# Kernel optimization log

Hardware: AMD Instinct MI355X
Metric: run time of the kernel (lower is better)

Reference implementation:

```python
import jax, jax.numpy as jnp
import numpy as np

IN_F = 1024
OUT_F = 2048
BATCH = 1024
LAMBD = 0.2
TOL = 1e-4
MAX_ITERS = 100


def setup_inputs() -> dict:
    key = jax.random.key(0)
    kx, kw = jax.random.split(key)
    x = jax.random.normal(kx, (BATCH, IN_F), dtype=jnp.float32)
    # weight init exactly as in torch __init__: randn then column-wise (dim=0) L2 normalization
    w = jax.random.normal(kw, (OUT_F, IN_F), dtype=jnp.float32)
    w = w / jnp.linalg.norm(w, axis=0)  # norm over out_features, broadcast over columns
    A = w.T  # (in, out)
    M = A.T @ A + jnp.eye(OUT_F, dtype=jnp.float32)  # (out, out)
    M_inv = jnp.linalg.inv(M).T
    return {"x": x, "weight": w, "M_inv": M_inv}


def _softshrink(z, lambd):
    return jnp.sign(z) * jnp.maximum(jnp.abs(z) - lambd, 0.0)


def _basis_pursuit_admm(A_dot_b, M_inv, lambd=LAMBD, tol=TOL, max_iters=MAX_ITERS):
    # Mask-based equivalent of the torch dynamic-resizing loop: solved rows are
    # frozen instead of removed; v_solution captures v at the iteration a row converges.
    B, Mdim = A_dot_b.shape
    z = jnp.zeros((B, Mdim), dtype=A_dot_b.dtype)
    solved0 = jnp.zeros((B,), dtype=bool)
    init = (z, z, z, z, solved0)  # v, u, v_prev, v_solution, solved

    def step(carry, _):
        v, u, v_prev, v_sol, solved = carry
        b_eff = A_dot_b + v - u                      # (B, M)
        xk = b_eff @ M_inv                           # (B, M) @ (M, M)
        v_new = _softshrink(xk + u, lambd)
        u_new = u + xk - v_new
        # negligible_improvement on the updated v vs previous v
        dx = jnp.linalg.norm(v_new - v_prev, axis=1)
        xn = jnp.linalg.norm(v_new, axis=1)
        conv = (dx / xn) < tol
        newly = conv & (~solved)
        v_sol = jnp.where(newly[:, None], v_new, v_sol)
        frozen = solved[:, None]
        v = jnp.where(frozen, v, v_new)
        u = jnp.where(frozen, u, u_new)
        solved = solved | newly
        return (v, u, v, v_sol, solved), None

    (v, u, v_prev, v_sol, solved), _ = jax.lax.scan(step, init, None, length=max_iters)
    # Matches torch: rows still unsolved after max_iters keep their initial zero solution.
    return v_sol


def reference(x, weight, M_inv):
    input_shape = x.shape
    b = jax.lax.stop_gradient(x.reshape(x.shape[0], -1))  # x.detach() in torch
    A_dot_b = b @ weight.T                                 # b.matmul(A) with A = weight.T
    encoded = _basis_pursuit_admm(A_dot_b, M_inv)
    decoded = encoded @ weight
    return encoded, decoded.reshape(input_shape)
```

## Files before the change

### kernel.cpp

```cpp
#include <hip/hip_runtime.h>
#include <math.h>

#define BATCH 1024
#define IN_F  1024
#define OUT_F 2048
#define LAMBD 0.2f
#define TOL   1e-4f
#define MAX_ITERS 100

#define KSPLIT 4
#define KCHUNK (OUT_F / KSPLIT)
#define BSCALE 32.0f
#define BSCALE_INV 0.03125f

typedef _Float16 half8 __attribute__((ext_vector_type(8)));
typedef _Float16 half4 __attribute__((ext_vector_type(4)));
typedef float    floatx16 __attribute__((ext_vector_type(16)));
typedef unsigned char fp8_t;

#define GLOAD_LDS16(g, l) __builtin_amdgcn_global_load_lds(              \
    (const __attribute__((address_space(1))) void*)(g),                  \
    (__attribute__((address_space(3))) void*)(l), 16, 0, 0)

__device__ inline int pk4_fp8(float a, float b, float c, float d) {
    int w = __builtin_amdgcn_cvt_pk_fp8_f32(a, b, 0, false);
    w = __builtin_amdgcn_cvt_pk_fp8_f32(c, d, w, true);
    return w;
}
__device__ inline fp8_t enc_fp8(float a) {
    return (fp8_t)(__builtin_amdgcn_cvt_pk_fp8_f32(a, a, 0, false) & 0xff);
}
__device__ inline void cvt4_fp8(int w, float o[4]) {
    o[0] = __builtin_amdgcn_cvt_f32_fp8(w, 0);
    o[1] = __builtin_amdgcn_cvt_f32_fp8(w, 1);
    o[2] = __builtin_amdgcn_cvt_f32_fp8(w, 2);
    o[3] = __builtin_amdgcn_cvt_f32_fp8(w, 3);
}

#define NB_INIT 2048
#define NB_CX   1024
#define NB_CW   2048
#define NB_TW   2048
#define NB_SB   4096
#define NB_TOTAL (NB_INIT + NB_CX + NB_CW + NB_TW + NB_SB)

__global__ __launch_bounds__(256)
void setup_kernel(const float* __restrict__ x, const float* __restrict__ w,
                  const float* __restrict__ Minv,
                  float4* __restrict__ v16, float4* __restrict__ u16,
                  float4* __restrict__ enc4, int* __restrict__ solved,
                  _Float16* __restrict__ xh, _Float16* __restrict__ wh,
                  _Float16* __restrict__ whT, fp8_t* __restrict__ BhT) {
    const int b = blockIdx.x;
    const int tid = threadIdx.x;
    __shared__ float tile[32][33];

    if (b < NB_INIT) {
        const int idx = b * 256 + tid;
        const float4 z = make_float4(0.f, 0.f, 0.f, 0.f);
        enc4[idx] = z;
        if (idx < BATCH * OUT_F / 8) { v16[idx] = z; u16[idx] = z; }
        if (idx < BATCH) solved[idx] = 0;
        return;
    }
    if (b < NB_INIT + NB_CX) {
        const int i = ((b - NB_INIT) * 256 + tid) * 4;
        const float4 f = *(const float4*)&x[i];
        half4 h;
        h[0] = (_Float16)f.x; h[1] = (_Float16)f.y;
        h[2] = (_Float16)f.z; h[3] = (_Float16)f.w;
        *(half4*)&xh[i] = h;
        return;
    }
    if (b < NB_INIT + NB_CX + NB_CW) {
        const int i = ((b - NB_INIT - NB_CX) * 256 + tid) * 4;
        const float4 f = *(const float4*)&w[i];
        half4 h;
        h[0] = (_Float16)f.x; h[1] = (_Float16)f.y;
        h[2] = (_Float16)f.z; h[3] = (_Float16)f.w;
        *(half4*)&wh[i] = h;
        return;
    }
    if (b < NB_INIT + NB_CX + NB_CW + NB_TW) {
        const int lb = b - NB_INIT - NB_CX - NB_CW;
        const int bx = lb & 31;
        const int by = lb >> 5;
        const int row0 = by * 32;
        const int col0 = bx * 32;
        const int r = tid >> 3;
        const int c4 = (tid & 7) * 4;
        const float4 b4 = *(const float4*)&w[(size_t)(row0 + r) * IN_F + col0 + c4];
        tile[r][c4 + 0] = b4.x; tile[r][c4 + 1] = b4.y;
        tile[r][c4 + 2] = b4.z; tile[r][c4 + 3] = b4.w;
        __syncthreads();
        half4 h;
#pragma unroll
        for (int j = 0; j < 4; ++j) h[j] = (_Float16)tile[c4 + j][r];
        *(half4*)&whT[(size_t)(col0 + r) * OUT_F + row0 + c4] = h;
        return;
    }
    {
        const int lb = b - NB_INIT - NB_CX - NB_CW - NB_TW;
        const int bx = lb & 63;
        const int by = lb >> 6;
        const int k0 = by * 32;
        const int n0 = bx * 32;
        const int r = tid >> 3;
        const int c4 = (tid & 7) * 4;
        const float4 b4 = *(const float4*)&Minv[(size_t)(k0 + r) * OUT_F + n0 + c4];
        tile[r][c4 + 0] = b4.x; tile[r][c4 + 1] = b4.y;
        tile[r][c4 + 2] = b4.z; tile[r][c4 + 3] = b4.w;
        __syncthreads();
        const int wrd = pk4_fp8(tile[c4 + 0][r] * BSCALE, tile[c4 + 1][r] * BSCALE,
                                tile[c4 + 2][r] * BSCALE, tile[c4 + 3][r] * BSCALE);
        *(int*)&BhT[(size_t)(n0 + r) * OUT_F + k0 + c4] = wrd;
    }
}

__global__ __launch_bounds__(256)
void cast_f16_kernel(const float* __restrict__ in, _Float16* __restrict__ out, int n) {
    const int i = (blockIdx.x * 256 + threadIdx.x) * 4;
    if (i < n) {
        const float4 f = *(const float4*)&in[i];
        half4 h;
        h[0] = (_Float16)f.x; h[1] = (_Float16)f.y;
        h[2] = (_Float16)f.z; h[3] = (_Float16)f.w;
        *(half4*)&out[i] = h;
    }
}

__global__ __launch_bounds__(256)
void mfma_nt_ab(const _Float16* __restrict__ A, const _Float16* __restrict__ B,
                fp8_t* __restrict__ Ab8, fp8_t* __restrict__ Ah,
                int N, int K) {
    __shared__ _Float16 sAB[2][8192];
    const int tid = threadIdx.x;
    const int m0 = blockIdx.y * 128;
    const int n0 = blockIdx.x * 128;
    const int wv = tid >> 6, ln = tid & 63;
    const int half = ln >> 5, l31 = ln & 31;
    const int wm = (wv >> 1) * 64, wn = (wv & 1) * 64;
    const int r0 = tid >> 2, koff = (tid & 3) * 8;
    const size_t ga0 = (size_t)(m0 + r0) * K + koff;
    const size_t ga1 = (size_t)(m0 + r0 + 64) * K + koff;
    const size_t gb0 = (size_t)(n0 + r0) * K + koff;
    const size_t gb1 = (size_t)(n0 + r0 + 64) * K + koff;
    const int ldst0 = tid * 8, ldst1 = (256 + tid) * 8;

    floatx16 acc[2][2];
#pragma unroll
    for (int a = 0; a < 2; ++a)
#pragma unroll
        for (int b = 0; b < 2; ++b)
#pragma unroll
            for (int q = 0; q < 16; ++q) acc[a][b][q] = 0.f;

    {
        _Float16* bufA = sAB[0];
        _Float16* bufB = sAB[0] + 4096;
        GLOAD_LDS16(A + ga0, bufA + ldst0);
        GLOAD_LDS16(A + ga1, bufA + ldst1);
        GLOAD_LDS16(B + gb0, bufB + ldst0);
        GLOAD_LDS16(B + gb1, bufB + ldst1);
    }
    __syncthreads();

    const int nsteps = K >> 5;
    for (int s = 0; s < nsteps; ++s) {
        const int cur = s & 1;
        if (s + 1 < nsteps) {
            const int k = (s + 1) * 32;
            _Float16* bufA = sAB[cur ^ 1];
            _Float16* bufB = sAB[cur ^ 1] + 4096;
            GLOAD_LDS16(A + ga0 + k, bufA + ldst0);
            GLOAD_LDS16(A + ga1 + k, bufA + ldst1);
            GLOAD_LDS16(B + gb0 + k, bufB + ldst0);
            GLOAD_LDS16(B + gb1 + k, bufB + ldst1);
        }
        const _Float16* sA = sAB[cur];
        const _Float16* sB = sAB[cur] + 4096;
#pragma unroll
        for (int kk = 0; kk < 2; ++kk) {
            const int ko = kk * 16 + half * 8;
            const half8 a0 = *(const half8*)&sA[(wm + l31) * 32 + ko];
            const half8 a1 = *(const half8*)&sA[(wm + 32 + l31) * 32 + ko];
            const half8 b0 = *(const half8*)&sB[(wn + l31) * 32 + ko];
            const half8 b1 = *(const half8*)&sB[(wn + 32 + l31) * 32 + ko];
            acc[0][0] = __builtin_amdgcn_mfma_f32_32x32x16_f16(a0, b0, acc[0][0], 0, 0, 0);
            acc[0][1] = __builtin_amdgcn_mfma_f32_32x32x16_f16(a0, b1, acc[0][1], 0, 0, 0);
            acc[1][0] = __builtin_amdgcn_mfma_f32_32x32x16_f16(a1, b0, acc[1][0], 0, 0, 0);
            acc[1][1] = __builtin_amdgcn_mfma_f32_32x32x16_f16(a1, b1, acc[1][1], 0, 0, 0);
        }
        __syncthreads();
    }
#pragma unroll
    for (int mm = 0; mm < 2; ++mm)
#pragma unroll
        for (int nn = 0; nn < 2; ++nn) {
            const int col = n0 + wn + nn * 32 + l31;
#pragma unroll
            for (int q = 0; q < 16; ++q) {
                const int row = m0 + wm + mm * 32 + (q & 3) + 8 * (q >> 2) + 4 * half;
                const size_t o = (size_t)row * N + col;
                const fp8_t e = enc_fp8(acc[mm][nn][q]);
                Ab8[o] = e;
                Ah[o] = e;
            }
        }
}

__global__ __launch_bounds__(256)
void mfma_nn_dec(const _Float16* __restrict__ A, const _Float16* __restrict__ B,
                 float* __restrict__ C, int N, int K) {
    __shared__ _Float16 sAB[2][8192];
    const int tid = threadIdx.x;
    const int m0 = blockIdx.y * 128;
    const int n0 = blockIdx.x * 128;
    const int wv = tid >> 6, ln = tid & 63;
    const int half = ln >> 5, l31 = ln & 31;
    const int wm = (wv >> 1) * 64, wn = (wv & 1) * 64;
    const int r0 = tid >> 2, koff = (tid & 3) * 8;
    const size_t ga0 = (size_t)(m0 + r0) * K + koff;
    const size_t ga1 = (size_t)(m0 + r0 + 64) * K + koff;
    const size_t gb0 = (size_t)(n0 + r0) * K + koff;
    const size_t gb1 = (size_t)(n0 + r0 + 64) * K + koff;
    const int ldst0 = tid * 8, ldst1 = (256 + tid) * 8;

    floatx16 acc[2][2];
#pragma unroll
    for (int a = 0; a < 2; ++a)
#pragma unroll
        for (int b = 0; b < 2; ++b)
#pragma unroll
            for (int q = 0; q < 16; ++q) acc[a][b][q] = 0.f;

    {
        _Float16* bufA = sAB[0];
        _Float16* bufB = sAB[0] + 4096;
        GLOAD_LDS16(A + ga0, bufA + ldst0);
        GLOAD_LDS16(A + ga1, bufA + ldst1);
        GLOAD_LDS16(B + gb0, bufB + ldst0);
        GLOAD_LDS16(B + gb1, bufB + ldst1);
    }
    __syncthreads();

    const int nsteps = K >> 5;
    for (int s = 0; s < nsteps; ++s) {
        const int cur = s & 1;
        if (s + 1 < nsteps) {
            const int k = (s + 1) * 32;
            _Float16* bufA = sAB[cur ^ 1];
            _Float16* bufB = sAB[cur ^ 1] + 4096;
            GLOAD_LDS16(A + ga0 + k, bufA + ldst0);
            GLOAD_LDS16(A + ga1 + k, bufA + ldst1);
            GLOAD_LDS16(B + gb0 + k, bufB + ldst0);
            GLOAD_LDS16(B + gb1 + k, bufB + ldst1);
        }
        const _Float16* sA = sAB[cur];
        const _Float16* sB = sAB[cur] + 4096;
#pragma unroll
        for (int kk = 0; kk < 2; ++kk) {
            const int ko = kk * 16 + half * 8;
            const half8 a0 = *(const half8*)&sA[(wm + l31) * 32 + ko];
            const half8 a1 = *(const half8*)&sA[(wm + 32 + l31) * 32 + ko];
            const half8 b0 = *(const half8*)&sB[(wn + l31) * 32 + ko];
            const half8 b1 = *(const half8*)&sB[(wn + 32 + l31) * 32 + ko];
            acc[0][0] = __builtin_amdgcn_mfma_f32_32x32x16_f16(a0, b0, acc[0][0], 0, 0, 0);
            acc[0][1] = __builtin_amdgcn_mfma_f32_32x32x16_f16(a0, b1, acc[0][1], 0, 0, 0);
            acc[1][0] = __builtin_amdgcn_mfma_f32_32x32x16_f16(a1, b0, acc[1][0], 0, 0, 0);
            acc[1][1] = __builtin_amdgcn_mfma_f32_32x32x16_f16(a1, b1, acc[1][1], 0, 0, 0);
        }
        __syncthreads();
    }
#pragma unroll
    for (int mm = 0; mm < 2; ++mm)
#pragma unroll
        for (int nn = 0; nn < 2; ++nn) {
            const int col = n0 + wn + nn * 32 + l31;
#pragma unroll
            for (int q = 0; q < 16; ++q) {
                const int row = m0 + wm + mm * 32 + (q & 3) + 8 * (q >> 2) + 4 * half;
                C[(size_t)row * N + col] = acc[mm][nn][q];
            }
        }
}

__global__ __launch_bounds__(256)
void xk_mfma(const fp8_t* __restrict__ Ah, const fp8_t* __restrict__ BhT,
             fp8_t* __restrict__ xkp, const int* __restrict__ solved) {
    __shared__ fp8_t smem[2][16384];
    const int tid = threadIdx.x;
    const int m0 = blockIdx.y * 128;
    const int n0 = blockIdx.x * 128;
    const int kz = blockIdx.z;
    constexpr size_t P = (size_t)BATCH * OUT_F;

    __shared__ int s_active;
    if (tid == 0) s_active = 0;
    __syncthreads();
    if (tid < 128 && solved[m0 + tid] == 0) s_active = 1;
    __syncthreads();
    if (!s_active) return;

    const int wv = tid >> 6;
    const int ln = tid & 63;
    const int half = ln >> 5;
    const int l31 = ln & 31;
    const int wm = (wv >> 1) * 64;
    const int wn = (wv & 1) * 64;

    const int r = tid & 127;
    const int c0 = tid >> 7;
    const fp8_t* gA = Ah  + (size_t)(m0 + r) * OUT_F + kz * KCHUNK;
    const fp8_t* gB = BhT + (size_t)(n0 + r) * OUT_F + kz * KCHUNK;
    const int dA0 = (c0 * 128 + r) * 16;
    const int dA1 = ((c0 + 2) * 128 + r) * 16;

    floatx16 acc[2][2];
#pragma unroll
    for (int a = 0; a < 2; ++a)
#pragma unroll
        for (int b = 0; b < 2; ++b)
#pragma unroll
            for (int q = 0; q < 16; ++q) acc[a][b][q] = 0.f;

    const int ao0 = (wm + l31) * 16 + half * 8;
    const int ao1 = (wm + 32 + l31) * 16 + half * 8;
    const int bo0 = (wn + l31) * 16 + half * 8;
    const int bo1 = (wn + 32 + l31) * 16 + half * 8;

    {
        fp8_t* sA = smem[0];
        fp8_t* sB = smem[0] + 8192;
        GLOAD_LDS16(gA + c0 * 16, sA + dA0);
        GLOAD_LDS16(gA + (c0 + 2) * 16, sA + dA1);
        GLOAD_LDS16(gB + c0 * 16, sB + dA0);
        GLOAD_LDS16(gB + (c0 + 2) * 16, sB + dA1);
    }
    __syncthreads();

#pragma unroll 1
    for (int s = 0; s < KCHUNK / 64; ++s) {
        const int cur = s & 1;
        if (s + 1 < KCHUNK / 64) {
            const int k = (s + 1) * 64;
            fp8_t* nA = smem[cur ^ 1];
            fp8_t* nB = smem[cur ^ 1] + 8192;
            GLOAD_LDS16(gA + k + c0 * 16, nA + dA0);
            GLOAD_LDS16(gA + k + (c0 + 2) * 16, nA + dA1);
            GLOAD_LDS16(gB + k + c0 * 16, nB + dA0);
            GLOAD_LDS16(gB + k + (c0 + 2) * 16, nB + dA1);
        }
        const fp8_t* sA = smem[cur];
        const fp8_t* sB = smem[cur] + 8192;
#pragma unroll
        for (int kk = 0; kk < 4; ++kk) {
            const int cb = kk * 2048;
            const long long a0 = *(const long long*)&sA[cb + ao0];
            const long long a1 = *(const long long*)&sA[cb + ao1];
            const long long b0 = *(const long long*)&sB[cb + bo0];
            const long long b1 = *(const long long*)&sB[cb + bo1];
            acc[0][0] = __builtin_amdgcn_mfma_f32_32x32x16_fp8_fp8(a0, b0, acc[0][0], 0, 0, 0);
            acc[0][1] = __builtin_amdgcn_mfma_f32_32x32x16_fp8_fp8(a0, b1, acc[0][1], 0, 0, 0);
            acc[1][0] = __builtin_amdgcn_mfma_f32_32x32x16_fp8_fp8(a1, b0, acc[1][0], 0, 0, 0);
            acc[1][1] = __builtin_amdgcn_mfma_f32_32x32x16_fp8_fp8(a1, b1, acc[1][1], 0, 0, 0);
        }
        __syncthreads();
    }

    fp8_t* sm = smem[0];
#pragma unroll
    for (int mm = 0; mm < 2; ++mm)
#pragma unroll
        for (int nn = 0; nn < 2; ++nn) {
            const int lcol = wn + nn * 32 + l31;
#pragma unroll
            for (int q = 0; q < 16; ++q) {
                const int lrow = wm + mm * 32 + (q & 3) + 8 * (q >> 2) + 4 * half;
                sm[lrow * 128 + lcol] = enc_fp8(acc[mm][nn][q] * BSCALE_INV);
            }
        }
    __syncthreads();
    fp8_t* outp = xkp + kz * P + (size_t)m0 * OUT_F + n0;
#pragma unroll
    for (int s4 = 0; s4 < 4; ++s4) {
        const int f = (s4 * 256 + tid) * 16;
        *(int4*)&outp[(size_t)(f >> 7) * OUT_F + (f & 127)] = *(const int4*)&sm[f];
    }
}

__global__ __launch_bounds__(256)
void update_kernel(const fp8_t* __restrict__ xkp, const fp8_t* __restrict__ Ab8,
                   _Float16* __restrict__ v, _Float16* __restrict__ u,
                   float* __restrict__ enc, fp8_t* __restrict__ Ah,
                   int* __restrict__ solved) {
    const int row = blockIdx.x;
    if (solved[row]) return;
    const int t = threadIdx.x;
    constexpr size_t P = (size_t)BATCH * OUT_F;

    const int c = t * 8;
    const size_t off = (size_t)row * OUT_F + c;
    const int2 q0 = *(const int2*)&xkp[off];
    const int2 q1 = *(const int2*)&xkp[P + off];
    const int2 q2 = *(const int2*)&xkp[2 * P + off];
    const int2 q3 = *(const int2*)&xkp[3 * P + off];
    const half8 u8 = *(const half8*)&u[off];
    const half8 v8 = *(const half8*)&v[off];
    const int2 ab2 = *(const int2*)&Ab8[off];

    float f0[4], f1[4], f2[4], f3[4], g0[4], g1[4], g2[4], g3[4];
    cvt4_fp8(q0.x, f0); cvt4_fp8(q1.x, f1); cvt4_fp8(q2.x, f2); cvt4_fp8(q3.x, f3);
    cvt4_fp8(q0.y, g0); cvt4_fp8(q1.y, g1); cvt4_fp8(q2.y, g2); cvt4_fp8(q3.y, g3);
    float ab0[4], ab1[4];
    cvt4_fp8(ab2.x, ab0); cvt4_fp8(ab2.y, ab1);
    float xs[8], abv[8];
#pragma unroll
    for (int j = 0; j < 4; ++j) {
        xs[j] = f0[j] + f1[j] + f2[j] + f3[j];
        xs[j + 4] = g0[j] + g1[j] + g2[j] + g3[j];
        abv[j] = ab0[j];
        abv[j + 4] = ab1[j];
    }

    float vn_all[8], ae[8];
    half8 vo, uo;
    float dx2 = 0.f, xn2 = 0.f;
#pragma unroll
    for (int j = 0; j < 8; ++j) {
        const float xk = xs[j];
        const float uv = (float)u8[j];
        const float vp = (float)v8[j];
        const float z = xk + uv;
        const float az = fabsf(z) - LAMBD;
        const float vnew = az > 0.f ? copysignf(az, z) : 0.f;
        const float unew = uv + xk - vnew;
        const float d = vnew - vp;
        dx2 += d * d;
        xn2 += vnew * vnew;
        vn_all[j] = vnew;
        vo[j] = (_Float16)vnew;
        uo[j] = (_Float16)unew;
        ae[j] = abv[j] + vnew - unew;
    }
    *(half8*)&v[off] = vo;
    *(half8*)&u[off] = uo;
    int2 ah;
    ah.x = pk4_fp8(ae[0], ae[1], ae[2], ae[3]);
    ah.y = pk4_fp8(ae[4], ae[5], ae[6], ae[7]);
    *(int2*)&Ah[off] = ah;

#pragma unroll
    for (int o = 32; o > 0; o >>= 1) {
        dx2 += __shfl_down(dx2, o);
        xn2 += __shfl_down(xn2, o);
    }
    __shared__ float sdx[4], sxn[4];
    __shared__ float s_conv;
    if ((t & 63) == 0) { sdx[t >> 6] = dx2; sxn[t >> 6] = xn2; }
    __syncthreads();
    if (t == 0) {
        const float dxt = sqrtf(sdx[0] + sdx[1] + sdx[2] + sdx[3]);
        const float xnt = sqrtf(sxn[0] + sxn[1] + sxn[2] + sxn[3]);
        const bool conv = (dxt / xnt) < TOL;
        s_conv = conv ? 1.f : 0.f;
        if (conv) solved[row] = 1;
    }
    __syncthreads();
    if (s_conv != 0.f) {
        *(float4*)&enc[off] = make_float4(vn_all[0], vn_all[1], vn_all[2], vn_all[3]);
        *(float4*)&enc[off + 4] = make_float4(vn_all[4], vn_all[5], vn_all[6], vn_all[7]);
    }
}

extern "C" void kernel_launch(void* const* d_in, const int* in_sizes, int n_in,
                              void* d_out, int out_size, void* d_ws, size_t ws_size,
                              hipStream_t stream) {
    (void)in_sizes; (void)n_in; (void)out_size; (void)ws_size;
    const float* x    = (const float*)d_in[0];
    const float* w    = (const float*)d_in[1];
    const float* Minv = (const float*)d_in[2];

    float* enc = (float*)d_out;
    float* dec = enc + (size_t)BATCH * OUT_F;

    constexpr size_t P = (size_t)BATCH * OUT_F;
    fp8_t* Ab8 = (fp8_t*)d_ws;
    _Float16* v   = (_Float16*)(Ab8 + P);
    _Float16* u   = v + P;
    _Float16* xh  = u + P;
    _Float16* wh  = xh + (size_t)BATCH * IN_F;
    _Float16* whT = wh + (size_t)OUT_F * IN_F;
    _Float16* ench = whT + (size_t)IN_F * OUT_F;
    fp8_t* Ah  = (fp8_t*)(ench + P);
    fp8_t* xkp = Ah + P;
    fp8_t* BhT = xkp + 4 * P;
    int* solved = (int*)(BhT + (size_t)OUT_F * OUT_F);

    setup_kernel<<<NB_TOTAL, 256, 0, stream>>>(
        x, w, Minv, (float4*)v, (float4*)u, (float4*)enc, solved,
        xh, wh, whT, BhT);

    mfma_nt_ab<<<dim3(OUT_F / 128, BATCH / 128), 256, 0, stream>>>(
        xh, wh, Ab8, Ah, OUT_F, IN_F);

    for (int it = 0; it < MAX_ITERS; ++it) {
        xk_mfma<<<dim3(OUT_F / 128, BATCH / 128, KSPLIT), 256, 0, stream>>>(
            Ah, BhT, xkp, solved);
        update_kernel<<<BATCH, 256, 0, stream>>>(xkp, Ab8, v, u, enc, Ah, solved);
    }

    cast_f16_kernel<<<(BATCH * OUT_F / 4 + 255) / 256, 256, 0, stream>>>(enc, ench, BATCH * OUT_F);
    mfma_nn_dec<<<dim3(IN_F / 128, BATCH / 128), 256, 0, stream>>>(
        ench, whT, dec, IN_F, OUT_F);
}
```

Baseline: 2.313 ms.

## Use 512-thread blocks with single-buffered LDS in the MFMA GEMM kernels

The three MFMA GEMM kernels (initial A·b, the per-iteration xk split-K GEMM, and decode) now run with 8 waves per block instead of 4. Each wave computes a 64x32 sub-tile with two accumulators rather than 64x64 with four, and the LDS double buffer is replaced by one buffer with a barrier before and after each load. The aim is more waves in flight to hide latency, and fewer registers and less shared memory per block. In exchange, global loads no longer overlap with MFMA work, each step takes two barriers, and each wave reuses fewer LDS fragments per load.

```diff
diff --git a/kernel.cpp b/kernel.cpp
--- a/kernel.cpp
+++ b/kernel.cpp
@@ -129,166 +129,112 @@
     }
 }
 
-__global__ __launch_bounds__(256)
+__global__ __launch_bounds__(512)
 void mfma_nt_ab(const _Float16* __restrict__ A, const _Float16* __restrict__ B,
                 fp8_t* __restrict__ Ab8, fp8_t* __restrict__ Ah,
                 int N, int K) {
-    __shared__ _Float16 sAB[2][8192];
+    __shared__ _Float16 sA[128 * 32];
+    __shared__ _Float16 sB[128 * 32];
     const int tid = threadIdx.x;
     const int m0 = blockIdx.y * 128;
     const int n0 = blockIdx.x * 128;
     const int wv = tid >> 6, ln = tid & 63;
     const int half = ln >> 5, l31 = ln & 31;
-    const int wm = (wv >> 1) * 64, wn = (wv & 1) * 64;
+    const int wm = (wv >> 2) * 64, wn = (wv & 3) * 32;
     const int r0 = tid >> 2, koff = (tid & 3) * 8;
     const size_t ga0 = (size_t)(m0 + r0) * K + koff;
-    const size_t ga1 = (size_t)(m0 + r0 + 64) * K + koff;
     const size_t gb0 = (size_t)(n0 + r0) * K + koff;
-    const size_t gb1 = (size_t)(n0 + r0 + 64) * K + koff;
-    const int ldst0 = tid * 8, ldst1 = (256 + tid) * 8;
-
-    floatx16 acc[2][2];
+    const int ldst = tid * 8;
+
+    floatx16 acc[2];
 #pragma unroll
     for (int a = 0; a < 2; ++a)
 #pragma unroll
-        for (int b = 0; b < 2; ++b)
-#pragma unroll
-            for (int q = 0; q < 16; ++q) acc[a][b][q] = 0.f;
-
-    {
-        _Float16* bufA = sAB[0];
-        _Float16* bufB = sAB[0] + 4096;
-        GLOAD_LDS16(A + ga0, bufA + ldst0);
-        GLOAD_LDS16(A + ga1, bufA + ldst1);
-        GLOAD_LDS16(B + gb0, bufB + ldst0);
-        GLOAD_LDS16(B + gb1, bufB + ldst1);
-    }
-    __syncthreads();
-
-    const int nsteps = K >> 5;
-    for (int s = 0; s < nsteps; ++s) {
-        const int cur = s & 1;
-        if (s + 1 < nsteps) {
-            const int k = (s + 1) * 32;
-            _Float16* bufA = sAB[cur ^ 1];
-            _Float16* bufB = sAB[cur ^ 1] + 4096;
-            GLOAD_LDS16(A + ga0 + k, bufA + ldst0);
-            GLOAD_LDS16(A + ga1 + k, bufA + ldst1);
-            GLOAD_LDS16(B + gb0 + k, bufB + ldst0);
-            GLOAD_LDS16(B + gb1 + k, bufB + ldst1);
-        }
-        const _Float16* sA = sAB[cur];
-        const _Float16* sB = sAB[cur] + 4096;
+        for (int q = 0; q < 16; ++q) acc[a][q] = 0.f;
+
+    for (int k = 0; k < K; k += 32) {
+        __syncthreads();
+        GLOAD_LDS16(A + ga0 + k, sA + ldst);
+        GLOAD_LDS16(B + gb0 + k, sB + ldst);
+        __syncthreads();
 #pragma unroll
         for (int kk = 0; kk < 2; ++kk) {
             const int ko = kk * 16 + half * 8;
             const half8 a0 = *(const half8*)&sA[(wm + l31) * 32 + ko];
             const half8 a1 = *(const half8*)&sA[(wm + 32 + l31) * 32 + ko];
             const half8 b0 = *(const half8*)&sB[(wn + l31) * 32 + ko];
-            const half8 b1 = *(const half8*)&sB[(wn + 32 + l31) * 32 + ko];
-            acc[0][0] = __builtin_amdgcn_mfma_f32_32x32x16_f16(a0, b0, acc[0][0], 0, 0, 0);
-            acc[0][1] = __builtin_amdgcn_mfma_f32_32x32x16_f16(a0, b1, acc[0][1], 0, 0, 0);
-            acc[1][0] = __builtin_amdgcn_mfma_f32_32x32x16_f16(a1, b0, acc[1][0], 0, 0, 0);
-            acc[1][1] = __builtin_amdgcn_mfma_f32_32x32x16_f16(a1, b1, acc[1][1], 0, 0, 0);
-        }
-        __syncthreads();
-    }
-#pragma unroll
-    for (int mm = 0; mm < 2; ++mm)
-#pragma unroll
-        for (int nn = 0; nn < 2; ++nn) {
-            const int col = n0 + wn + nn * 32 + l31;
-#pragma unroll
-            for (int q = 0; q < 16; ++q) {
-                const int row = m0 + wm + mm * 32 + (q & 3) + 8 * (q >> 2) + 4 * half;
-                const size_t o = (size_t)row * N + col;
-                const fp8_t e = enc_fp8(acc[mm][nn][q]);
-                Ab8[o] = e;
-                Ah[o] = e;
-            }
-        }
-}
-
-__global__ __launch_bounds__(256)
+            acc[0] = __builtin_amdgcn_mfma_f32_32x32x16_f16(a0, b0, acc[0], 0, 0, 0);
+            acc[1] = __builtin_amdgcn_mfma_f32_32x32x16_f16(a1, b0, acc[1], 0, 0, 0);
+        }
+    }
+#pragma unroll
+    for (int mm = 0; mm < 2; ++mm) {
+        const int col = n0 + wn + l31;
+#pragma unroll
+        for (int q = 0; q < 16; ++q) {
+            const int row = m0 + wm + mm * 32 + (q & 3) + 8 * (q >> 2) + 4 * half;
+            const size_t o = (size_t)row * N + col;
+            const fp8_t e = enc_fp8(acc[mm][q]);
+            Ab8[o] = e;
+            Ah[o] = e;
+        }
+    }
+}
+
+__global__ __launch_bounds__(512)
 void mfma_nn_dec(const _Float16* __restrict__ A, const _Float16* __restrict__ B,
                  float* __restrict__ C, int N, int K) {
-    __shared__ _Float16 sAB[2][8192];
+    __shared__ _Float16 sA[128 * 32];
+    __shared__ _Float16 sB[128 * 32];
     const int tid = threadIdx.x;
     const int m0 = blockIdx.y * 128;
     const int n0 = blockIdx.x * 128;
     const int wv = tid >> 6, ln = tid & 63;
     const int half = ln >> 5, l31 = ln & 31;
-    const int wm = (wv >> 1) * 64, wn = (wv & 1) * 64;
+    const int wm = (wv >> 2) * 64, wn = (wv & 3) * 32;
     const int r0 = tid >> 2, koff = (tid & 3) * 8;
     const size_t ga0 = (size_t)(m0 + r0) * K + koff;
-    const size_t ga1 = (size_t)(m0 + r0 + 64) * K + koff;
     const size_t gb0 = (size_t)(n0 + r0) * K + koff;
-    const size_t gb1 = (size_t)(n0 + r0 + 64) * K + koff;
-    const int ldst0 = tid * 8, ldst1 = (256 + tid) * 8;
-
-    floatx16 acc[2][2];
+    const int ldst = tid * 8;
+
+    floatx16 acc[2];
 #pragma unroll
     for (int a = 0; a < 2; ++a)
 #pragma unroll
-        for (int b = 0; b < 2; ++b)
-#pragma unroll
-            for (int q = 0; q < 16; ++q) acc[a][b][q] = 0.f;
-
-    {
-        _Float16* bufA = sAB[0];
-        _Float16* bufB = sAB[0] + 4096;
-        GLOAD_LDS16(A + ga0, bufA + ldst0);
-        GLOAD_LDS16(A + ga1, bufA + ldst1);
-        GLOAD_LDS16(B + gb0, bufB + ldst0);
-        GLOAD_LDS16(B + gb1, bufB + ldst1);
-    }
-    __syncthreads();
-
-    const int nsteps = K >> 5;
-    for (int s = 0; s < nsteps; ++s) {
-        const int cur = s & 1;
-        if (s + 1 < nsteps) {
-            const int k = (s + 1) * 32;
-            _Float16* bufA = sAB[cur ^ 1];
-            _Float16* bufB = sAB[cur ^ 1] + 4096;
-            GLOAD_LDS16(A + ga0 + k, bufA + ldst0);
-            GLOAD_LDS16(A + ga1 + k, bufA + ldst1);
-            GLOAD_LDS16(B + gb0 + k, bufB + ldst0);
-            GLOAD_LDS16(B + gb1 + k, bufB + ldst1);
-        }
-        const _Float16* sA = sAB[cur];
-        const _Float16* sB = sAB[cur] + 4096;
+        for (int q = 0; q < 16; ++q) acc[a][q] = 0.f;
+
+    for (int k = 0; k < K; k += 32) {
+        __syncthreads();
+        GLOAD_LDS16(A + ga0 + k, sA + ldst);
+        GLOAD_LDS16(B + gb0 + k, sB + ldst);
+        __syncthreads();
 #pragma unroll
         for (int kk = 0; kk < 2; ++kk) {
             const int ko = kk * 16 + half * 8;
             const half8 a0 = *(const half8*)&sA[(wm + l31) * 32 + ko];
             const half8 a1 = *(const half8*)&sA[(wm + 32 + l31) * 32 + ko];
             const half8 b0 = *(const half8*)&sB[(wn + l31) * 32 + ko];
-            const half8 b1 = *(const half8*)&sB[(wn + 32 + l31) * 32 + ko];
-            acc[0][0] = __builtin_amdgcn_mfma_f32_32x32x16_f16(a0, b0, acc[0][0], 0, 0, 0);
-            acc[0][1] = __builtin_amdgcn_mfma_f32_32x32x16_f16(a0, b1, acc[0][1], 0, 0, 0);
-            acc[1][0] = __builtin_amdgcn_mfma_f32_32x32x16_f16(a1, b0, acc[1][0], 0, 0, 0);
-            acc[1][1] = __builtin_amdgcn_mfma_f32_32x32x16_f16(a1, b1, acc[1][1], 0, 0, 0);
-        }
-        __syncthreads();
-    }
-#pragma unroll
-    for (int mm = 0; mm < 2; ++mm)
-#pragma unroll
-        for (int nn = 0; nn < 2; ++nn) {
-            const int col = n0 + wn + nn * 32 + l31;
-#pragma unroll
-            for (int q = 0; q < 16; ++q) {
-                const int row = m0 + wm + mm * 32 + (q & 3) + 8 * (q >> 2) + 4 * half;
-                C[(size_t)row * N + col] = acc[mm][nn][q];
-            }
-        }
-}
-
-__global__ __launch_bounds__(256)
+            acc[0] = __builtin_amdgcn_mfma_f32_32x32x16_f16(a0, b0, acc[0], 0, 0, 0);
+            acc[1] = __builtin_amdgcn_mfma_f32_32x32x16_f16(a1, b0, acc[1], 0, 0, 0);
+        }
+    }
+#pragma unroll
+    for (int mm = 0; mm < 2; ++mm) {
+        const int col = n0 + wn + l31;
+#pragma unroll
+        for (int q = 0; q < 16; ++q) {
+            const int row = m0 + wm + mm * 32 + (q & 3) + 8 * (q >> 2) + 4 * half;
+            C[(size_t)row * N + col] = acc[mm][q];
+        }
+    }
+}
+
+__global__ __launch_bounds__(512)
 void xk_mfma(const fp8_t* __restrict__ Ah, const fp8_t* __restrict__ BhT,
              fp8_t* __restrict__ xkp, const int* __restrict__ solved) {
-    __shared__ fp8_t smem[2][16384];
+    __shared__ fp8_t smem[16384];
+    fp8_t* sA = smem;
+    fp8_t* sB = smem + 8192;
     const int tid = threadIdx.x;
     const int m0 = blockIdx.y * 128;
     const int n0 = blockIdx.x * 128;
@@ -306,86 +252,58 @@
     const int ln = tid & 63;
     const int half = ln >> 5;
     const int l31 = ln & 31;
-    const int wm = (wv >> 1) * 64;
-    const int wn = (wv & 1) * 64;
+    const int wm = (wv >> 2) * 64;
+    const int wn = (wv & 3) * 32;
 
     const int r = tid & 127;
     const int c0 = tid >> 7;
     const fp8_t* gA = Ah  + (size_t)(m0 + r) * OUT_F + kz * KCHUNK;
     const fp8_t* gB = BhT + (size_t)(n0 + r) * OUT_F + kz * KCHUNK;
-    const int dA0 = (c0 * 128 + r) * 16;
-    const int dA1 = ((c0 + 2) * 128 + r) * 16;
-
-    floatx16 acc[2][2];
+    const int dst = (c0 * 128 + r) * 16;
+
+    floatx16 acc[2];
 #pragma unroll
     for (int a = 0; a < 2; ++a)
 #pragma unroll
-        for (int b = 0; b < 2; ++b)
-#pragma unroll
-            for (int q = 0; q < 16; ++q) acc[a][b][q] = 0.f;
+        for (int q = 0; q < 16; ++q) acc[a][q] = 0.f;
 
     const int ao0 = (wm + l31) * 16 + half * 8;
     const int ao1 = (wm + 32 + l31) * 16 + half * 8;
     const int bo0 = (wn + l31) * 16 + half * 8;
-    const int bo1 = (wn + 32 + l31) * 16 + half * 8;
-
-    {
-        fp8_t* sA = smem[0];
-        fp8_t* sB = smem[0] + 8192;
-        GLOAD_LDS16(gA + c0 * 16, sA + dA0);
-        GLOAD_LDS16(gA + (c0 + 2) * 16, sA + dA1);
-        GLOAD_LDS16(gB + c0 * 16, sB + dA0);
-        GLOAD_LDS16(gB + (c0 + 2) * 16, sB + dA1);
-    }
-    __syncthreads();
-
-#pragma unroll 1
-    for (int s = 0; s < KCHUNK / 64; ++s) {
-        const int cur = s & 1;
-        if (s + 1 < KCHUNK / 64) {
-            const int k = (s + 1) * 64;
-            fp8_t* nA = smem[cur ^ 1];
-            fp8_t* nB = smem[cur ^ 1] + 8192;
-            GLOAD_LDS16(gA + k + c0 * 16, nA + dA0);
-            GLOAD_LDS16(gA + k + (c0 + 2) * 16, nA + dA1);
-            GLOAD_LDS16(gB + k + c0 * 16, nB + dA0);
-            GLOAD_LDS16(gB + k + (c0 + 2) * 16, nB + dA1);
-        }
-        const fp8_t* sA = smem[cur];
-        const fp8_t* sB = smem[cur] + 8192;
+
+    for (int k = 0; k < KCHUNK; k += 64) {
+        __syncthreads();
+        GLOAD_LDS16(gA + k + c0 * 16, sA + dst);
+        GLOAD_LDS16(gB + k + c0 * 16, sB + dst);
+        __syncthreads();
+
 #pragma unroll
         for (int kk = 0; kk < 4; ++kk) {
             const int cb = kk * 2048;
             const long long a0 = *(const long long*)&sA[cb + ao0];
             const long long a1 = *(const long long*)&sA[cb + ao1];
             const long long b0 = *(const long long*)&sB[cb + bo0];
-            const long long b1 = *(const long long*)&sB[cb + bo1];
-            acc[0][0] = __builtin_amdgcn_mfma_f32_32x32x16_fp8_fp8(a0, b0, acc[0][0], 0, 0, 0);
-            acc[0][1] = __builtin_amdgcn_mfma_f32_32x32x16_fp8_fp8(a0, b1, acc[0][1], 0, 0, 0);
-            acc[1][0] = __builtin_amdgcn_mfma_f32_32x32x16_fp8_fp8(a1, b0, acc[1][0], 0, 0, 0);
-            acc[1][1] = __builtin_amdgcn_mfma_f32_32x32x16_fp8_fp8(a1, b1, acc[1][1], 0, 0, 0);
-        }
-        __syncthreads();
-    }
-
-    fp8_t* sm = smem[0];
-#pragma unroll
-    for (int mm = 0; mm < 2; ++mm)
-#pragma unroll
-        for (int nn = 0; nn < 2; ++nn) {
-            const int lcol = wn + nn * 32 + l31;
-#pragma unroll
-            for (int q = 0; q < 16; ++q) {
-                const int lrow = wm + mm * 32 + (q & 3) + 8 * (q >> 2) + 4 * half;
-                sm[lrow * 128 + lcol] = enc_fp8(acc[mm][nn][q] * BSCALE_INV);
-            }
-        }
+            acc[0] = __builtin_amdgcn_mfma_f32_32x32x16_fp8_fp8(a0, b0, acc[0], 0, 0, 0);
+            acc[1] = __builtin_amdgcn_mfma_f32_32x32x16_fp8_fp8(a1, b0, acc[1], 0, 0, 0);
+        }
+    }
+
+    __syncthreads();
+#pragma unroll
+    for (int mm = 0; mm < 2; ++mm) {
+        const int lcol = wn + l31;
+#pragma unroll
+        for (int q = 0; q < 16; ++q) {
+            const int lrow = wm + mm * 32 + (q & 3) + 8 * (q >> 2) + 4 * half;
+            smem[lrow * 128 + lcol] = enc_fp8(acc[mm][q] * BSCALE_INV);
+        }
+    }
     __syncthreads();
     fp8_t* outp = xkp + kz * P + (size_t)m0 * OUT_F + n0;
 #pragma unroll
-    for (int s4 = 0; s4 < 4; ++s4) {
-        const int f = (s4 * 256 + tid) * 16;
-        *(int4*)&outp[(size_t)(f >> 7) * OUT_F + (f & 127)] = *(const int4*)&sm[f];
+    for (int s4 = 0; s4 < 2; ++s4) {
+        const int f = (s4 * 512 + tid) * 16;
+        *(int4*)&outp[(size_t)(f >> 7) * OUT_F + (f & 127)] = *(const int4*)&smem[f];
     }
 }
 
@@ -501,16 +419,16 @@
         x, w, Minv, (float4*)v, (float4*)u, (float4*)enc, solved,
         xh, wh, whT, BhT);
 
-    mfma_nt_ab<<<dim3(OUT_F / 128, BATCH / 128), 256, 0, stream>>>(
+    mfma_nt_ab<<<dim3(OUT_F / 128, BATCH / 128), 512, 0, stream>>>(
         xh, wh, Ab8, Ah, OUT_F, IN_F);
 
     for (int it = 0; it < MAX_ITERS; ++it) {
-        xk_mfma<<<dim3(OUT_F / 128, BATCH / 128, KSPLIT), 256, 0, stream>>>(
+        xk_mfma<<<dim3(OUT_F / 128, BATCH / 128, KSPLIT), 512, 0, stream>>>(
             Ah, BhT, xkp, solved);
         update_kernel<<<BATCH, 256, 0, stream>>>(xkp, Ab8, v, u, enc, Ah, solved);
     }
 
     cast_f16_kernel<<<(BATCH * OUT_F / 4 + 255) / 256, 256, 0, stream>>>(enc, ench, BATCH * OUT_F);
-    mfma_nn_dec<<<dim3(IN_F / 128, BATCH / 128), 256, 0, stream>>>(
+    mfma_nn_dec<<<dim3(IN_F / 128, BATCH / 128), 512, 0, stream>>>(
         ench, whT, dec, IN_F, OUT_F);
 }
```

Measured after the change: 2.315 ms. About the same (+0.1%).

## Fuse ADMM matmul and update into one kernel with deferred convergence check

Applied to the files above, without the earlier changes.

Merges the split-K FP8 matmul and the per-row update into one kernel. Each 128x128 tile now covers the full K range and applies softshrink, the u/v updates and the next A operand directly from an LDS float tile. This removes the fp8 partial-sum round trip through global memory and one launch per iteration. Row convergence norms become per-tile partials in a ping-pong buffer that the next iteration checks, plus a finalize kernel and a zeroing cast for unsolved rows. The cost is only 128 blocks with no split-K, a single-buffered K loop with two barriers per step, and enc written on every iteration.

```diff
diff --git a/kernel.cpp b/kernel.cpp
--- a/kernel.cpp
+++ b/kernel.cpp
@@ -8,10 +8,9 @@
 #define TOL   1e-4f
 #define MAX_ITERS 100
 
-#define KSPLIT 4
-#define KCHUNK (OUT_F / KSPLIT)
 #define BSCALE 32.0f
 #define BSCALE_INV 0.03125f
+#define PNHALF (BATCH * 32)
 
 typedef _Float16 half8 __attribute__((ext_vector_type(8)));
 typedef _Float16 half4 __attribute__((ext_vector_type(4)));
@@ -49,6 +48,7 @@
                   const float* __restrict__ Minv,
                   float4* __restrict__ v16, float4* __restrict__ u16,
                   float4* __restrict__ enc4, int* __restrict__ solved,
+                  float4* __restrict__ pn4,
                   _Float16* __restrict__ xh, _Float16* __restrict__ wh,
                   _Float16* __restrict__ whT, fp8_t* __restrict__ BhT) {
     const int b = blockIdx.x;
@@ -61,6 +61,7 @@
         enc4[idx] = z;
         if (idx < BATCH * OUT_F / 8) { v16[idx] = z; u16[idx] = z; }
         if (idx < BATCH) solved[idx] = 0;
+        if (idx < 2 * PNHALF / 4) pn4[idx] = z;
         return;
     }
     if (b < NB_INIT + NB_CX) {
@@ -118,22 +119,10 @@
 }
 
 __global__ __launch_bounds__(256)
-void cast_f16_kernel(const float* __restrict__ in, _Float16* __restrict__ out, int n) {
-    const int i = (blockIdx.x * 256 + threadIdx.x) * 4;
-    if (i < n) {
-        const float4 f = *(const float4*)&in[i];
-        half4 h;
-        h[0] = (_Float16)f.x; h[1] = (_Float16)f.y;
-        h[2] = (_Float16)f.z; h[3] = (_Float16)f.w;
-        *(half4*)&out[i] = h;
-    }
-}
-
-__global__ __launch_bounds__(256)
 void mfma_nt_ab(const _Float16* __restrict__ A, const _Float16* __restrict__ B,
                 fp8_t* __restrict__ Ab8, fp8_t* __restrict__ Ah,
                 int N, int K) {
-    __shared__ _Float16 sAB[2][8192];
+    __shared__ _Float16 smem[2][8192];
     const int tid = threadIdx.x;
     const int m0 = blockIdx.y * 128;
     const int n0 = blockIdx.x * 128;
@@ -155,30 +144,26 @@
 #pragma unroll
             for (int q = 0; q < 16; ++q) acc[a][b][q] = 0.f;
 
-    {
-        _Float16* bufA = sAB[0];
-        _Float16* bufB = sAB[0] + 4096;
-        GLOAD_LDS16(A + ga0, bufA + ldst0);
-        GLOAD_LDS16(A + ga1, bufA + ldst1);
-        GLOAD_LDS16(B + gb0, bufB + ldst0);
-        GLOAD_LDS16(B + gb1, bufB + ldst1);
-    }
+    GLOAD_LDS16(A + ga0, smem[0] + ldst0);
+    GLOAD_LDS16(A + ga1, smem[0] + ldst1);
+    GLOAD_LDS16(B + gb0, smem[0] + 4096 + ldst0);
+    GLOAD_LDS16(B + gb1, smem[0] + 4096 + ldst1);
     __syncthreads();
 
-    const int nsteps = K >> 5;
-    for (int s = 0; s < nsteps; ++s) {
-        const int cur = s & 1;
-        if (s + 1 < nsteps) {
+    const int NS = K >> 5;
+#pragma unroll 1
+    for (int s = 0; s < NS; ++s) {
+        if (s + 1 < NS) {
+            _Float16* nb = smem[(s & 1) ^ 1];
             const int k = (s + 1) * 32;
-            _Float16* bufA = sAB[cur ^ 1];
-            _Float16* bufB = sAB[cur ^ 1] + 4096;
-            GLOAD_LDS16(A + ga0 + k, bufA + ldst0);
-            GLOAD_LDS16(A + ga1 + k, bufA + ldst1);
-            GLOAD_LDS16(B + gb0 + k, bufB + ldst0);
-            GLOAD_LDS16(B + gb1 + k, bufB + ldst1);
-        }
-        const _Float16* sA = sAB[cur];
-        const _Float16* sB = sAB[cur] + 4096;
+            GLOAD_LDS16(A + ga0 + k, nb + ldst0);
+            GLOAD_LDS16(A + ga1 + k, nb + ldst1);
+            GLOAD_LDS16(B + gb0 + k, nb + 4096 + ldst0);
+            GLOAD_LDS16(B + gb1 + k, nb + 4096 + ldst1);
+        }
+        __syncthreads();
+        const _Float16* sA = smem[s & 1];
+        const _Float16* sB = smem[s & 1] + 4096;
 #pragma unroll
         for (int kk = 0; kk < 2; ++kk) {
             const int ko = kk * 16 + half * 8;
@@ -212,7 +197,7 @@
 __global__ __launch_bounds__(256)
 void mfma_nn_dec(const _Float16* __restrict__ A, const _Float16* __restrict__ B,
                  float* __restrict__ C, int N, int K) {
-    __shared__ _Float16 sAB[2][8192];
+    __shared__ _Float16 smem[2][8192];
     const int tid = threadIdx.x;
     const int m0 = blockIdx.y * 128;
     const int n0 = blockIdx.x * 128;
@@ -234,30 +219,26 @@
 #pragma unroll
             for (int q = 0; q < 16; ++q) acc[a][b][q] = 0.f;
 
-    {
-        _Float16* bufA = sAB[0];
-        _Float16* bufB = sAB[0] + 4096;
-        GLOAD_LDS16(A + ga0, bufA + ldst0);
-        GLOAD_LDS16(A + ga1, bufA + ldst1);
-        GLOAD_LDS16(B + gb0, bufB + ldst0);
-        GLOAD_LDS16(B + gb1, bufB + ldst1);
-    }
+    GLOAD_LDS16(A + ga0, smem[0] + ldst0);
+    GLOAD_LDS16(A + ga1, smem[0] + ldst1);
+    GLOAD_LDS16(B + gb0, smem[0] + 4096 + ldst0);
+    GLOAD_LDS16(B + gb1, smem[0] + 4096 + ldst1);
     __syncthreads();
 
-    const int nsteps = K >> 5;
-    for (int s = 0; s < nsteps; ++s) {
-        const int cur = s & 1;
-        if (s + 1 < nsteps) {
+    const int NS = K >> 5;
+#pragma unroll 1
+    for (int s = 0; s < NS; ++s) {
+        if (s + 1 < NS) {
+            _Float16* nb = smem[(s & 1) ^ 1];
             const int k = (s + 1) * 32;
-            _Float16* bufA = sAB[cur ^ 1];
-            _Float16* bufB = sAB[cur ^ 1] + 4096;
-            GLOAD_LDS16(A + ga0 + k, bufA + ldst0);
-            GLOAD_LDS16(A + ga1 + k, bufA + ldst1);
-            GLOAD_LDS16(B + gb0 + k, bufB + ldst0);
-            GLOAD_LDS16(B + gb1 + k, bufB + ldst1);
-        }
-        const _Float16* sA = sAB[cur];
-        const _Float16* sB = sAB[cur] + 4096;
+            GLOAD_LDS16(A + ga0 + k, nb + ldst0);
+            GLOAD_LDS16(A + ga1 + k, nb + ldst1);
+            GLOAD_LDS16(B + gb0 + k, nb + 4096 + ldst0);
+            GLOAD_LDS16(B + gb1 + k, nb + 4096 + ldst1);
+        }
+        __syncthreads();
+        const _Float16* sA = smem[s & 1];
+        const _Float16* sB = smem[s & 1] + 4096;
 #pragma unroll
         for (int kk = 0; kk < 2; ++kk) {
             const int ko = kk * 16 + half * 8;
@@ -286,19 +267,45 @@
 }
 
 __global__ __launch_bounds__(256)
-void xk_mfma(const fp8_t* __restrict__ Ah, const fp8_t* __restrict__ BhT,
-             fp8_t* __restrict__ xkp, const int* __restrict__ solved) {
-    __shared__ fp8_t smem[2][16384];
+void fused_iter(const fp8_t* __restrict__ AhCur, fp8_t* __restrict__ AhNxt,
+                const fp8_t* __restrict__ BhT, const fp8_t* __restrict__ Ab8,
+                _Float16* __restrict__ v, _Float16* __restrict__ u,
+                float* __restrict__ enc, int* __restrict__ solved,
+                const float* __restrict__ pnPrev, float* __restrict__ pnCur) {
+    __shared__ __align__(16) fp8_t smem[65536];
+    __shared__ int s_flags[128];
+    __shared__ int s_active;
+
     const int tid = threadIdx.x;
-    const int m0 = blockIdx.y * 128;
-    const int n0 = blockIdx.x * 128;
-    const int kz = blockIdx.z;
-    constexpr size_t P = (size_t)BATCH * OUT_F;
-
-    __shared__ int s_active;
+    const int bx = blockIdx.x;
+    const int by = blockIdx.y;
+    const int m0 = by * 128;
+    const int n0 = bx * 128;
+
     if (tid == 0) s_active = 0;
     __syncthreads();
-    if (tid < 128 && solved[m0 + tid] == 0) s_active = 1;
+    if (tid < 128) {
+        const int row = m0 + tid;
+        int act = 0;
+        if (solved[row] == 0) {
+            const float* pp = pnPrev + row * 32;
+            float dx2 = 0.f, xn2 = 0.f;
+#pragma unroll
+            for (int j = 0; j < 16; ++j) { dx2 += pp[2 * j]; xn2 += pp[2 * j + 1]; }
+            const bool conv = (sqrtf(dx2) / sqrtf(xn2)) < TOL;
+            if (conv) {
+                solved[row] = 1;
+                const int4* src = (const int4*)(AhCur + (size_t)row * OUT_F + n0);
+                int4* dst = (int4*)(AhNxt + (size_t)row * OUT_F + n0);
+#pragma unroll
+                for (int j = 0; j < 8; ++j) dst[j] = src[j];
+            } else {
+                act = 1;
+                s_active = 1;
+            }
+        }
+        s_flags[tid] = act;
+    }
     __syncthreads();
     if (!s_active) return;
 
@@ -311,10 +318,12 @@
 
     const int r = tid & 127;
     const int c0 = tid >> 7;
-    const fp8_t* gA = Ah  + (size_t)(m0 + r) * OUT_F + kz * KCHUNK;
-    const fp8_t* gB = BhT + (size_t)(n0 + r) * OUT_F + kz * KCHUNK;
-    const int dA0 = (c0 * 128 + r) * 16;
-    const int dA1 = ((c0 + 2) * 128 + r) * 16;
+    const fp8_t* gA = AhCur + (size_t)(m0 + r) * OUT_F;
+    const fp8_t* gB = BhT + (size_t)(n0 + r) * OUT_F;
+    const int d0 = ((c0 + 0) * 128 + r) * 16;
+    const int d1 = ((c0 + 2) * 128 + r) * 16;
+    const int d2 = ((c0 + 4) * 128 + r) * 16;
+    const int d3 = ((c0 + 6) * 128 + r) * 16;
 
     floatx16 acc[2][2];
 #pragma unroll
@@ -329,46 +338,35 @@
     const int bo0 = (wn + l31) * 16 + half * 8;
     const int bo1 = (wn + 32 + l31) * 16 + half * 8;
 
-    {
-        fp8_t* sA = smem[0];
-        fp8_t* sB = smem[0] + 8192;
-        GLOAD_LDS16(gA + c0 * 16, sA + dA0);
-        GLOAD_LDS16(gA + (c0 + 2) * 16, sA + dA1);
-        GLOAD_LDS16(gB + c0 * 16, sB + dA0);
-        GLOAD_LDS16(gB + (c0 + 2) * 16, sB + dA1);
-    }
-    __syncthreads();
-
 #pragma unroll 1
-    for (int s = 0; s < KCHUNK / 64; ++s) {
-        const int cur = s & 1;
-        if (s + 1 < KCHUNK / 64) {
-            const int k = (s + 1) * 64;
-            fp8_t* nA = smem[cur ^ 1];
-            fp8_t* nB = smem[cur ^ 1] + 8192;
-            GLOAD_LDS16(gA + k + c0 * 16, nA + dA0);
-            GLOAD_LDS16(gA + k + (c0 + 2) * 16, nA + dA1);
-            GLOAD_LDS16(gB + k + c0 * 16, nB + dA0);
-            GLOAD_LDS16(gB + k + (c0 + 2) * 16, nB + dA1);
-        }
-        const fp8_t* sA = smem[cur];
-        const fp8_t* sB = smem[cur] + 8192;
-#pragma unroll
-        for (int kk = 0; kk < 4; ++kk) {
+    for (int kb = 0; kb < OUT_F / 128; ++kb) {
+        const int ko = kb * 128;
+        __syncthreads();
+        GLOAD_LDS16(gA + ko + (c0 + 0) * 16, smem + d0);
+        GLOAD_LDS16(gA + ko + (c0 + 2) * 16, smem + d1);
+        GLOAD_LDS16(gA + ko + (c0 + 4) * 16, smem + d2);
+        GLOAD_LDS16(gA + ko + (c0 + 6) * 16, smem + d3);
+        GLOAD_LDS16(gB + ko + (c0 + 0) * 16, smem + 16384 + d0);
+        GLOAD_LDS16(gB + ko + (c0 + 2) * 16, smem + 16384 + d1);
+        GLOAD_LDS16(gB + ko + (c0 + 4) * 16, smem + 16384 + d2);
+        GLOAD_LDS16(gB + ko + (c0 + 6) * 16, smem + 16384 + d3);
+        __syncthreads();
+#pragma unroll
+        for (int kk = 0; kk < 8; ++kk) {
             const int cb = kk * 2048;
-            const long long a0 = *(const long long*)&sA[cb + ao0];
-            const long long a1 = *(const long long*)&sA[cb + ao1];
-            const long long b0 = *(const long long*)&sB[cb + bo0];
-            const long long b1 = *(const long long*)&sB[cb + bo1];
+            const long long a0 = *(const long long*)&smem[cb + ao0];
+            const long long a1 = *(const long long*)&smem[cb + ao1];
+            const long long b0 = *(const long long*)&smem[16384 + cb + bo0];
+            const long long b1 = *(const long long*)&smem[16384 + cb + bo1];
             acc[0][0] = __builtin_amdgcn_mfma_f32_32x32x16_fp8_fp8(a0, b0, acc[0][0], 0, 0, 0);
             acc[0][1] = __builtin_amdgcn_mfma_f32_32x32x16_fp8_fp8(a0, b1, acc[0][1], 0, 0, 0);
             acc[1][0] = __builtin_amdgcn_mfma_f32_32x32x16_fp8_fp8(a1, b0, acc[1][0], 0, 0, 0);
             acc[1][1] = __builtin_amdgcn_mfma_f32_32x32x16_fp8_fp8(a1, b1, acc[1][1], 0, 0, 0);
         }
-        __syncthreads();
-    }
-
-    fp8_t* sm = smem[0];
+    }
+
+    __syncthreads();
+    float* ftile = (float*)smem;
 #pragma unroll
     for (int mm = 0; mm < 2; ++mm)
 #pragma unroll
@@ -377,100 +375,92 @@
 #pragma unroll
             for (int q = 0; q < 16; ++q) {
                 const int lrow = wm + mm * 32 + (q & 3) + 8 * (q >> 2) + 4 * half;
-                sm[lrow * 128 + lcol] = enc_fp8(acc[mm][nn][q] * BSCALE_INV);
+                ftile[lrow * 128 + (lcol ^ (lrow & 31))] = acc[mm][nn][q] * BSCALE_INV;
             }
         }
     __syncthreads();
-    fp8_t* outp = xkp + kz * P + (size_t)m0 * OUT_F + n0;
-#pragma unroll
-    for (int s4 = 0; s4 < 4; ++s4) {
-        const int f = (s4 * 256 + tid) * 16;
-        *(int4*)&outp[(size_t)(f >> 7) * OUT_F + (f & 127)] = *(const int4*)&sm[f];
+
+    const int urow = tid >> 1;
+    if (s_flags[urow]) {
+        const int row = m0 + urow;
+        const int cb = (tid & 1) * 64;
+        const size_t off = (size_t)row * OUT_F + n0 + cb;
+        const float* ft = ftile + urow * 128;
+        const int rx = urow & 31;
+        float dx2 = 0.f, xn2 = 0.f;
+#pragma unroll
+        for (int j8 = 0; j8 < 8; ++j8) {
+            const size_t o8 = off + j8 * 8;
+            const half8 u8 = *(const half8*)&u[o8];
+            const half8 v8 = *(const half8*)&v[o8];
+            const int2 ab2 = *(const int2*)&Ab8[o8];
+            float ab[8];
+            cvt4_fp8(ab2.x, ab); cvt4_fp8(ab2.y, ab + 4);
+            half8 vo, uo;
+            float vn[8], ae[8];
+#pragma unroll
+            for (int j = 0; j < 8; ++j) {
+                const float xk = ft[(cb + j8 * 8 + j) ^ rx];
+                const float uv = (float)u8[j];
+                const float vp = (float)v8[j];
+                const float z = xk + uv;
+                const float az = fabsf(z) - LAMBD;
+                const float vnew = az > 0.f ? copysignf(az, z) : 0.f;
+                const float unew = uv + xk - vnew;
+                const float d = vnew - vp;
+                dx2 += d * d;
+                xn2 += vnew * vnew;
+                vn[j] = vnew;
+                vo[j] = (_Float16)vnew;
+                uo[j] = (_Float16)unew;
+                ae[j] = ab[j] + vnew - unew;
+            }
+            *(half8*)&v[o8] = vo;
+            *(half8*)&u[o8] = uo;
+            int2 ah;
+            ah.x = pk4_fp8(ae[0], ae[1], ae[2], ae[3]);
+            ah.y = pk4_fp8(ae[4], ae[5], ae[6], ae[7]);
+            *(int2*)&AhNxt[o8] = ah;
+            *(float4*)&enc[o8] = make_float4(vn[0], vn[1], vn[2], vn[3]);
+            *(float4*)&enc[o8 + 4] = make_float4(vn[4], vn[5], vn[6], vn[7]);
+        }
+        dx2 += __shfl_xor(dx2, 1);
+        xn2 += __shfl_xor(xn2, 1);
+        if ((tid & 1) == 0) {
+            pnCur[row * 32 + bx * 2] = dx2;
+            pnCur[row * 32 + bx * 2 + 1] = xn2;
+        }
     }
 }
 
 __global__ __launch_bounds__(256)
-void update_kernel(const fp8_t* __restrict__ xkp, const fp8_t* __restrict__ Ab8,
-                   _Float16* __restrict__ v, _Float16* __restrict__ u,
-                   float* __restrict__ enc, fp8_t* __restrict__ Ah,
-                   int* __restrict__ solved) {
-    const int row = blockIdx.x;
-    if (solved[row]) return;
-    const int t = threadIdx.x;
-    constexpr size_t P = (size_t)BATCH * OUT_F;
-
-    const int c = t * 8;
-    const size_t off = (size_t)row * OUT_F + c;
-    const int2 q0 = *(const int2*)&xkp[off];
-    const int2 q1 = *(const int2*)&xkp[P + off];
-    const int2 q2 = *(const int2*)&xkp[2 * P + off];
-    const int2 q3 = *(const int2*)&xkp[3 * P + off];
-    const half8 u8 = *(const half8*)&u[off];
-    const half8 v8 = *(const half8*)&v[off];
-    const int2 ab2 = *(const int2*)&Ab8[off];
-
-    float f0[4], f1[4], f2[4], f3[4], g0[4], g1[4], g2[4], g3[4];
-    cvt4_fp8(q0.x, f0); cvt4_fp8(q1.x, f1); cvt4_fp8(q2.x, f2); cvt4_fp8(q3.x, f3);
-    cvt4_fp8(q0.y, g0); cvt4_fp8(q1.y, g1); cvt4_fp8(q2.y, g2); cvt4_fp8(q3.y, g3);
-    float ab0[4], ab1[4];
-    cvt4_fp8(ab2.x, ab0); cvt4_fp8(ab2.y, ab1);
-    float xs[8], abv[8];
-#pragma unroll
-    for (int j = 0; j < 4; ++j) {
-        xs[j] = f0[j] + f1[j] + f2[j] + f3[j];
-        xs[j + 4] = g0[j] + g1[j] + g2[j] + g3[j];
-        abv[j] = ab0[j];
-        abv[j + 4] = ab1[j];
-    }
-
-    float vn_all[8], ae[8];
-    half8 vo, uo;
-    float dx2 = 0.f, xn2 = 0.f;
-#pragma unroll
-    for (int j = 0; j < 8; ++j) {
-        const float xk = xs[j];
-        const float uv = (float)u8[j];
-        const float vp = (float)v8[j];
-        const float z = xk + uv;
-        const float az = fabsf(z) - LAMBD;
-        const float vnew = az > 0.f ? copysignf(az, z) : 0.f;
-        const float unew = uv + xk - vnew;
-        const float d = vnew - vp;
-        dx2 += d * d;
-        xn2 += vnew * vnew;
-        vn_all[j] = vnew;
-        vo[j] = (_Float16)vnew;
-        uo[j] = (_Float16)unew;
-        ae[j] = abv[j] + vnew - unew;
-    }
-    *(half8*)&v[off] = vo;
-    *(half8*)&u[off] = uo;
-    int2 ah;
-    ah.x = pk4_fp8(ae[0], ae[1], ae[2], ae[3]);
-    ah.y = pk4_fp8(ae[4], ae[5], ae[6], ae[7]);
-    *(int2*)&Ah[off] = ah;
-
-#pragma unroll
-    for (int o = 32; o > 0; o >>= 1) {
-        dx2 += __shfl_down(dx2, o);
-        xn2 += __shfl_down(xn2, o);
-    }
-    __shared__ float sdx[4], sxn[4];
-    __shared__ float s_conv;
-    if ((t & 63) == 0) { sdx[t >> 6] = dx2; sxn[t >> 6] = xn2; }
-    __syncthreads();
-    if (t == 0) {
-        const float dxt = sqrtf(sdx[0] + sdx[1] + sdx[2] + sdx[3]);
-        const float xnt = sqrtf(sxn[0] + sxn[1] + sxn[2] + sxn[3]);
-        const bool conv = (dxt / xnt) < TOL;
-        s_conv = conv ? 1.f : 0.f;
-        if (conv) solved[row] = 1;
-    }
-    __syncthreads();
-    if (s_conv != 0.f) {
-        *(float4*)&enc[off] = make_float4(vn_all[0], vn_all[1], vn_all[2], vn_all[3]);
-        *(float4*)&enc[off + 4] = make_float4(vn_all[4], vn_all[5], vn_all[6], vn_all[7]);
-    }
+void finalize_kernel(const float* __restrict__ pn, int* __restrict__ solved) {
+    const int row = blockIdx.x * 256 + threadIdx.x;
+    if (row < BATCH && solved[row] == 0) {
+        const float* pp = pn + row * 32;
+        float dx2 = 0.f, xn2 = 0.f;
+#pragma unroll
+        for (int j = 0; j < 16; ++j) { dx2 += pp[2 * j]; xn2 += pp[2 * j + 1]; }
+        if ((sqrtf(dx2) / sqrtf(xn2)) < TOL) solved[row] = 1;
+    }
+}
+
+__global__ __launch_bounds__(256)
+void cast_zero_kernel(float* __restrict__ enc, _Float16* __restrict__ out,
+                      const int* __restrict__ solved) {
+    const int i = (blockIdx.x * 256 + threadIdx.x) * 4;
+    const int row = i >> 11;
+    float4 f;
+    if (solved[row]) {
+        f = *(const float4*)&enc[i];
+    } else {
+        f = make_float4(0.f, 0.f, 0.f, 0.f);
+        *(float4*)&enc[i] = f;
+    }
+    half4 h;
+    h[0] = (_Float16)f.x; h[1] = (_Float16)f.y;
+    h[2] = (_Float16)f.z; h[3] = (_Float16)f.w;
+    *(half4*)&out[i] = h;
 }
 
 extern "C" void kernel_launch(void* const* d_in, const int* in_sizes, int n_in,
@@ -492,25 +482,32 @@
     _Float16* wh  = xh + (size_t)BATCH * IN_F;
     _Float16* whT = wh + (size_t)OUT_F * IN_F;
     _Float16* ench = whT + (size_t)IN_F * OUT_F;
-    fp8_t* Ah  = (fp8_t*)(ench + P);
-    fp8_t* xkp = Ah + P;
-    fp8_t* BhT = xkp + 4 * P;
+    fp8_t* Ah0 = (fp8_t*)(ench + P);
+    fp8_t* Ah1 = Ah0 + P;
+    float* pnorm = (float*)(Ah1 + P);
+    fp8_t* BhT = Ah0 + 5 * P;
     int* solved = (int*)(BhT + (size_t)OUT_F * OUT_F);
 
     setup_kernel<<<NB_TOTAL, 256, 0, stream>>>(
         x, w, Minv, (float4*)v, (float4*)u, (float4*)enc, solved,
-        xh, wh, whT, BhT);
+        (float4*)pnorm, xh, wh, whT, BhT);
 
     mfma_nt_ab<<<dim3(OUT_F / 128, BATCH / 128), 256, 0, stream>>>(
-        xh, wh, Ab8, Ah, OUT_F, IN_F);
-
+        xh, wh, Ab8, Ah0, OUT_F, IN_F);
+
+    fp8_t* ahb[2] = { Ah0, Ah1 };
     for (int it = 0; it < MAX_ITERS; ++it) {
-        xk_mfma<<<dim3(OUT_F / 128, BATCH / 128, KSPLIT), 256, 0, stream>>>(
-            Ah, BhT, xkp, solved);
-        update_kernel<<<BATCH, 256, 0, stream>>>(xkp, Ab8, v, u, enc, Ah, solved);
-    }
-
-    cast_f16_kernel<<<(BATCH * OUT_F / 4 + 255) / 256, 256, 0, stream>>>(enc, ench, BATCH * OUT_F);
+        const int p0 = it & 1, p1 = (it + 1) & 1;
+        fused_iter<<<dim3(16, 8), 256, 0, stream>>>(
+            ahb[p0], ahb[p1], BhT, Ab8, v, u, enc, solved,
+            pnorm + (size_t)p1 * PNHALF,
+            pnorm + (size_t)p0 * PNHALF);
+    }
+    finalize_kernel<<<(BATCH + 255) / 256, 256, 0, stream>>>(
+        pnorm + (size_t)((MAX_ITERS - 1) & 1) * PNHALF, solved);
+
+    cast_zero_kernel<<<(BATCH * OUT_F / 4 + 255) / 256, 256, 0, stream>>>(
+        enc, ench, solved);
     mfma_nn_dec<<<dim3(IN_F / 128, BATCH / 128), 256, 0, stream>>>(
         ench, whT, dec, IN_F, OUT_F);
 }
```

Result: slower. 4.810 ms (+108.0%).
